# Optimization experiments

Hardware: AMD Instinct MI355X
Metric: run time of the kernel (lower is better)

Reference implementation:

```python
import jax, jax.numpy as jnp
import numpy as np

BS = 8        # number of batched graphs (paired point clouds, must be even)
NPTS = 16384  # points per graph (equal-size graphs -> segment ops are per-row softmax)
C = 32        # feature channels
CG = 8        # global feature channels from pooling head
K = 256
KNN = 16      # key_mean_num neighbors


def setup_inputs() -> dict:
    key = jax.random.key(0)
    ks = jax.random.split(key, 5)
    N = BS * NPTS
    return {
        "feature": jax.random.normal(ks[0], (N, C, 1), dtype=jnp.float32),
        "pos": jax.random.normal(ks[1], (N, 3), dtype=jnp.float32),
        "W_pool": jax.random.normal(ks[2], (C, 1 + CG), dtype=jnp.float32) / np.float32(np.sqrt(C)),
        "W_regress": jax.random.normal(ks[3], (3 * C + 2 * CG, K), dtype=jnp.float32) / np.float32(np.sqrt(3 * C + 2 * CG)),
        "W_extract": jax.random.normal(ks[4], (C, C), dtype=jnp.float32) / np.float32(np.sqrt(C)),
        "bs": BS,
    }


def reference(feature, pos, W_pool, W_regress, W_extract, bs):
    N, Cc, _ = feature.shape
    n = N // bs
    f = feature.reshape(bs, n, Cc)          # [bs, n, C] (deg-0 fiber, D=1)
    pos_b = pos.reshape(bs, n, 3)

    # --- global pooling head: per-graph segment softmax (dgl.softmax_nodes) ---
    logits = jnp.einsum('bnc,cl->bnl', f, W_pool)      # [bs, n, 1+Cg]
    prob = jax.nn.softmax(logits[..., 0], axis=1)      # [bs, n] pooling weights
    batched = jnp.einsum('bnc,bn->bc', f, prob)        # dgl.sum_nodes weighted -> [bs, C]
    glob = jnp.einsum('bnl,bn->bl', logits[..., 1:], prob)  # [bs, Cg]

    # --- cat_0 cross-pair global merge (tensor_1 <-> tensor_2 swap) ---
    h = bs // 2
    extra = jnp.concatenate([jnp.concatenate([glob[:h], glob[h:]], 1),
                             jnp.concatenate([glob[h:], glob[:h]], 1)], 0)     # [bs, 2Cg]
    paired = jnp.concatenate([jnp.concatenate([batched[:h], batched[h:]], 1),
                              jnp.concatenate([batched[h:], batched[:h]], 1)], 0)  # [bs, 2C]
    f_new = jnp.concatenate([
        f,
        jnp.broadcast_to(extra[:, None, :], (bs, n, extra.shape[1])),   # broadcast_nodes
        jnp.broadcast_to(paired[:, None, :], (bs, n, paired.shape[1])),
    ], axis=-1)                                                          # [bs, n, 3C+2Cg]

    pw = jax.nn.softmax(jnp.einsum('bnc,ck->bnk', f_new, W_regress), axis=1)  # [bs, n, K]
    keypoints = jnp.einsum('bnk,bnd->bkd', pw, pos_b)                         # [bs, K, 3]

    # --- batched KNN: k nearest source points per keypoint, within graph ---
    d2 = jnp.sum((keypoints[:, :, None, :] - pos_b[:, None, :, :]) ** 2, axis=-1)  # [bs, K, n]
    _, idx = jax.lax.top_k(-d2, KNN)                                               # [bs, K, k]

    # --- bipartite gather + keypoint feature extraction (mean aggregate + linear) ---
    neigh = jax.vmap(lambda fb, ib: fb[ib])(f, idx)   # [bs, K, k, C]
    pooled = neigh.mean(axis=2)                        # [bs, K, C]
    return jnp.einsum('bkc,co->bko', pooled, W_extract)  # key_tensor [bs, K, C]
```

## Files before the change

### kernel.cpp

```cpp
#include <hip/hip_runtime.h>
#include <math.h>

#define BS 8
#define NPTS 16384
#define C 32
#define K 256
#define KNNK 16
#define NBINS 512
#define BINW 0.00025f
#define CAP 4096
#define NSPL 64

typedef float f32x4 __attribute__((ext_vector_type(4)));
typedef __bf16 bf16x8 __attribute__((ext_vector_type(8)));
union U16x8 { int4 i; bf16x8 v; unsigned short u[8]; };

__global__ __launch_bounds__(256, 2) void k_logits(
    const float* __restrict__ f, const float* __restrict__ pos,
    const float* __restrict__ Wr, float* __restrict__ partials) {
  int b = blockIdx.x >> 6;
  int r = blockIdx.x & 63;
  int pbase = b * NPTS + r * 256;
  int t = threadIdx.x;
  int w = t >> 6, lane = t & 63;
  int h = w & 1, nh = w >> 1;
  int quad = lane >> 4, col = lane & 15;

  __shared__ float4 posLDS[256];
  __shared__ float4 fm[2][256];

  float* rawf = (float*)&fm[0][0];
  if (t < 192) ((float4*)rawf)[t] = ((const float4*)(pos + (size_t)pbase * 3))[t];
  __syncthreads();
  float4 myp = make_float4(rawf[t * 3], rawf[t * 3 + 1], rawf[t * 3 + 2], 0.f);
  __syncthreads();
  posLDS[t] = myp;

  U16x8 Bh[8], Bl[8];
#pragma unroll
  for (int jt = 0; jt < 8; jt++) {
    int tile = h * 8 + jt;
#pragma unroll
    for (int j = 0; j < 8; j++) {
      float v = Wr[(quad * 8 + j) * K + tile * 16 + col];
      unsigned u = __float_as_uint(v);
      unsigned hb = u >> 16;
      float hf = __uint_as_float(hb << 16);
      unsigned lb = __float_as_uint(v - hf) >> 16;
      Bh[jt].u[j] = (unsigned short)hb;
      Bl[jt].u[j] = (unsigned short)lb;
    }
  }
  float acce[8], accx[8], accy[8], accz[8];
#pragma unroll
  for (int jt = 0; jt < 8; jt++) { acce[jt] = 0.f; accx[jt] = 0.f; accy[jt] = 0.f; accz[jt] = 0.f; }

#pragma unroll 1
  for (int nt = nh * 8; nt < nh * 8 + 8; nt++) {
    const float* fb = f + ((size_t)(pbase + nt * 16 + col)) * C + quad * 8;
    float4 a0 = *(const float4*)fb;
    float4 a1 = *(const float4*)(fb + 4);
    float av[8] = {a0.x, a0.y, a0.z, a0.w, a1.x, a1.y, a1.z, a1.w};
    U16x8 Ah, Al;
#pragma unroll
    for (int j = 0; j < 8; j++) {
      unsigned u = __float_as_uint(av[j]);
      unsigned hb = u >> 16;
      float hf = __uint_as_float(hb << 16);
      unsigned lb = __float_as_uint(av[j] - hf) >> 16;
      Ah.u[j] = (unsigned short)hb;
      Al.u[j] = (unsigned short)lb;
    }
    float4 pr0 = posLDS[nt * 16 + quad * 4 + 0];
    float4 pr1 = posLDS[nt * 16 + quad * 4 + 1];
    float4 pr2 = posLDS[nt * 16 + quad * 4 + 2];
    float4 pr3 = posLDS[nt * 16 + quad * 4 + 3];
#pragma unroll
    for (int jt = 0; jt < 8; jt++) {
      f32x4 d = {0.f, 0.f, 0.f, 0.f};
      d = __builtin_amdgcn_mfma_f32_16x16x32_bf16(Al.v, Bh[jt].v, d, 0, 0, 0);
      d = __builtin_amdgcn_mfma_f32_16x16x32_bf16(Ah.v, Bl[jt].v, d, 0, 0, 0);
      d = __builtin_amdgcn_mfma_f32_16x16x32_bf16(Ah.v, Bh[jt].v, d, 0, 0, 0);
      float e0 = __expf(d[0]), e1 = __expf(d[1]), e2 = __expf(d[2]), e3 = __expf(d[3]);
      acce[jt] += (e0 + e1) + (e2 + e3);
      accx[jt] += e0 * pr0.x + e1 * pr1.x + e2 * pr2.x + e3 * pr3.x;
      accy[jt] += e0 * pr0.y + e1 * pr1.y + e2 * pr2.y + e3 * pr3.y;
      accz[jt] += e0 * pr0.z + e1 * pr1.z + e2 * pr2.z + e3 * pr3.z;
    }
  }

#pragma unroll
  for (int jt = 0; jt < 8; jt++) {
    acce[jt] += __shfl_xor(acce[jt], 16); acce[jt] += __shfl_xor(acce[jt], 32);
    accx[jt] += __shfl_xor(accx[jt], 16); accx[jt] += __shfl_xor(accx[jt], 32);
    accy[jt] += __shfl_xor(accy[jt], 16); accy[jt] += __shfl_xor(accy[jt], 32);
    accz[jt] += __shfl_xor(accz[jt], 16); accz[jt] += __shfl_xor(accz[jt], 32);
  }
  __syncthreads();
  if (lane < 16) {
#pragma unroll
    for (int jt = 0; jt < 8; jt++)
      fm[nh][h * 128 + jt * 16 + lane] = make_float4(acce[jt], accx[jt], accy[jt], accz[jt]);
  }
  __syncthreads();
  float4 v0 = fm[0][t], v1 = fm[1][t];
  float4* po = (float4*)partials;
  po[(size_t)blockIdx.x * 256 + t] =
      make_float4(v0.x + v1.x, v0.y + v1.y, v0.z + v1.z, v0.w + v1.w);
}

__global__ __launch_bounds__(1024) void k_graph(
    const float* __restrict__ pos, const float* __restrict__ partials,
    int* __restrict__ knn) {
  int b = blockIdx.x;
  int t = threadIdx.x;
  int lane = t & 63, wave = t >> 6;

  __shared__ float4 mred[4][256];
  __shared__ float kxs[256], kys[256], kzs[256];
  __shared__ float wred[16][3];
  __shared__ float bc[6];
  __shared__ unsigned hist[NBINS];
  __shared__ unsigned lcnt, ovf;
  __shared__ float cxs[CAP], cys[CAP], czs[CAP];
  __shared__ int cis[CAP];

  {
    int kp = t & 255, q = t >> 8;
    const float4* po = (const float4*)partials;
    float sl = 0.f, sx = 0.f, sy = 0.f, sz = 0.f;
#pragma unroll 4
    for (int j = 0; j < 16; j++) {
      float4 v = po[((size_t)(b * NSPL + q * 16 + j)) * 256 + kp];
      sl += v.x; sx += v.y; sy += v.z; sz += v.w;
    }
    mred[q][kp] = make_float4(sl, sx, sy, sz);
  }
  for (int i = t; i < NBINS; i += 1024) hist[i] = 0;
  if (t == 0) { lcnt = 0; ovf = 0; }
  __syncthreads();
  if (t < 256) {
    float4 a0 = mred[0][t], a1 = mred[1][t], a2 = mred[2][t], a3 = mred[3][t];
    float L = (a0.x + a1.x) + (a2.x + a3.x);
    float inv = 1.f / L;
    kxs[t] = ((a0.y + a1.y) + (a2.y + a3.y)) * inv;
    kys[t] = ((a0.z + a1.z) + (a2.z + a3.z)) * inv;
    kzs[t] = ((a0.w + a1.w) + (a2.w + a3.w)) * inv;
  }
  __syncthreads();

  float sx = 0.f, sy = 0.f, sz = 0.f;
  if (t < 256) { sx = kxs[t]; sy = kys[t]; sz = kzs[t]; }
#pragma unroll
  for (int off = 32; off; off >>= 1) {
    sx += __shfl_xor(sx, off, 64);
    sy += __shfl_xor(sy, off, 64);
    sz += __shfl_xor(sz, off, 64);
  }
  if (lane == 0) { wred[wave][0] = sx; wred[wave][1] = sy; wred[wave][2] = sz; }
  __syncthreads();
  if (t == 0) {
    float X = 0.f, Y = 0.f, Z = 0.f;
#pragma unroll
    for (int i = 0; i < 16; i++) { X += wred[i][0]; Y += wred[i][1]; Z += wred[i][2]; }
    bc[0] = X / K; bc[1] = Y / K; bc[2] = Z / K;
  }
  __syncthreads();
  float cx = bc[0], cy = bc[1], cz = bc[2];
  float md = 0.f;
  if (t < 256) {
    float dx = kxs[t] - cx, dy = kys[t] - cy, dz = kzs[t] - cz;
    md = dx * dx + dy * dy + dz * dz;
  }
#pragma unroll
  for (int off = 32; off; off >>= 1) md = fmaxf(md, __shfl_xor(md, off, 64));
  if (lane == 0) wred[wave][0] = md;
  __syncthreads();
  if (t == 0) {
    float m = 0.f;
#pragma unroll
    for (int i = 0; i < 16; i++) m = fmaxf(m, wred[i][0]);
    bc[3] = sqrtf(m);
  }
  __syncthreads();

#pragma unroll 4
  for (int i = 0; i < 16; i++) {
    int p = b * NPTS + i * 1024 + t;
    float dx = pos[p * 3 + 0] - cx, dy = pos[p * 3 + 1] - cy, dz = pos[p * 3 + 2] - cz;
    float d2 = dx * dx + dy * dy + dz * dz;
    int bin = (int)(d2 * (1.0f / BINW));
    if (bin < NBINS - 1) atomicAdd(&hist[bin], 1u);
  }
  __syncthreads();

  if (t == 0) {
    unsigned cum = 0; float T2 = -1.f;
    for (int i = 0; i < NBINS - 1; i++) {
      cum += hist[i];
      if (cum >= KNNK) { T2 = (i + 1) * BINW; break; }
    }
    if (T2 < 0.f) bc[4] = 3.0e38f;
    else {
      float Rf = sqrtf(T2) + 2.f * bc[3];
      bc[4] = Rf * Rf;
    }
  }
  __syncthreads();
  float r2 = bc[4];

#pragma unroll 4
  for (int i = 0; i < 16; i++) {
    int pl = i * 1024 + t;
    int p = b * NPTS + pl;
    float px = pos[p * 3 + 0], py = pos[p * 3 + 1], pz = pos[p * 3 + 2];
    float dx = px - cx, dy = py - cy, dz = pz - cz;
    float d2 = dx * dx + dy * dy + dz * dz;
    if (d2 <= r2) {
      unsigned u = atomicAdd(&lcnt, 1u);
      if (u < CAP) { cxs[u] = px; cys[u] = py; czs[u] = pz; cis[u] = pl; }
      else ovf = 1;
    }
  }
  __syncthreads();

  if (t < 256) {
    float kx = kxs[t], ky = kys[t], kz = kzs[t];
    float dd[KNNK]; int ii[KNNK];
#pragma unroll
    for (int j = 0; j < KNNK; j++) { dd[j] = 1e30f; ii[j] = 0; }
    float mx = 1e30f;
    if (!ovf) {
      int n = (int)lcnt;
      for (int j = 0; j < n; j++) {
        float dx = kx - cxs[j], dy = ky - cys[j], dz = kz - czs[j];
        float d2 = dx * dx + dy * dy + dz * dz;
        if (d2 < mx) {
          int sm = 0; float bv = dd[0];
#pragma unroll
          for (int s = 1; s < KNNK; s++) if (dd[s] > bv) { bv = dd[s]; sm = s; }
#pragma unroll
          for (int s = 0; s < KNNK; s++) if (s == sm) { dd[s] = d2; ii[s] = cis[j]; }
          mx = dd[0];
#pragma unroll
          for (int s = 1; s < KNNK; s++) mx = fmaxf(mx, dd[s]);
        }
      }
    } else {
      for (int j = 0; j < NPTS; j++) {
        const float* pp = pos + (size_t)(b * NPTS + j) * 3;
        float dx = kx - pp[0], dy = ky - pp[1], dz = kz - pp[2];
        float d2 = dx * dx + dy * dy + dz * dz;
        if (d2 < mx) {
          int sm = 0; float bv = dd[0];
#pragma unroll
          for (int s = 1; s < KNNK; s++) if (dd[s] > bv) { bv = dd[s]; sm = s; }
#pragma unroll
          for (int s = 0; s < KNNK; s++) if (s == sm) { dd[s] = d2; ii[s] = j; }
          mx = dd[0];
#pragma unroll
          for (int s = 1; s < KNNK; s++) mx = fmaxf(mx, dd[s]);
        }
      }
    }
    for (int j = 0; j < KNNK; j++) knn[((size_t)(b * K + t)) * KNNK + j] = ii[j];
  }
}

__global__ __launch_bounds__(256) void k_extract(
    const float* __restrict__ f, const int* __restrict__ knn,
    const float* __restrict__ We, float* __restrict__ out) {
  __shared__ float P[8][C + 1];
  int tid = threadIdx.x;
  int kp = tid >> 5, c = tid & 31;
  int gk = blockIdx.x * 8 + kp;
  int b = gk >> 8;
  float s = 0.f;
#pragma unroll
  for (int j = 0; j < KNNK; j++) {
    int pl = knn[(size_t)gk * KNNK + j];
    s += f[((size_t)(b * NPTS + pl)) * C + c];
  }
  P[kp][c] = s * (1.f / KNNK);
  __syncthreads();
  float r = 0.f;
#pragma unroll
  for (int cc = 0; cc < C; cc++) r += P[kp][cc] * We[cc * C + c];
  out[(size_t)gk * C + c] = r;
}

extern "C" void kernel_launch(void* const* d_in, const int* in_sizes, int n_in,
                              void* d_out, int out_size, void* d_ws, size_t ws_size,
                              hipStream_t stream) {
  const float* f   = (const float*)d_in[0];
  const float* pos = (const float*)d_in[1];
  const float* Wr  = (const float*)d_in[3];
  const float* We  = (const float*)d_in[4];
  float* out = (float*)d_out;

  char* ws = (char*)d_ws;
  float* partials = (float*)(ws + 0);
  int*   knn      = (int*)(ws + (size_t)2 * 1024 * 1024);

  k_logits <<<dim3(BS * NSPL), dim3(256),  0, stream>>>(f, pos, Wr, partials);
  k_graph  <<<dim3(BS),        dim3(1024), 0, stream>>>(pos, partials, knn);
  k_extract<<<dim3(256),       dim3(256),  0, stream>>>(f, knn, We, out);
}
```

Before: 132.8 us.

## Split monolithic graph kernel into merge, histogram, compaction and top-k kernels

The single 8-block k_graph kernel becomes four kernels. Keypoint merging stays at 8 blocks, the distance histogram and candidate compaction now run on 64 blocks each through global atomics, and the top-k scan runs per graph with 256 threads. The goal is to spread the pos-scanning phases across more CUs instead of 8 workgroups. In exchange it adds three launches, global atomic contention, and a round trip for the candidate list through global memory.

```diff
diff --git a/kernel.cpp b/kernel.cpp
--- a/kernel.cpp
+++ b/kernel.cpp
@@ -109,9 +109,10 @@
       make_float4(v0.x + v1.x, v0.y + v1.y, v0.z + v1.z, v0.w + v1.w);
 }
 
-__global__ __launch_bounds__(1024) void k_graph(
-    const float* __restrict__ pos, const float* __restrict__ partials,
-    int* __restrict__ knn) {
+__global__ __launch_bounds__(1024) void k_merge(
+    const float* __restrict__ partials, float* __restrict__ kpts,
+    float* __restrict__ gstat, unsigned* __restrict__ ghist,
+    unsigned* __restrict__ ccnt) {
   int b = blockIdx.x;
   int t = threadIdx.x;
   int lane = t & 63, wave = t >> 6;
@@ -119,33 +120,32 @@
   __shared__ float4 mred[4][256];
   __shared__ float kxs[256], kys[256], kzs[256];
   __shared__ float wred[16][3];
-  __shared__ float bc[6];
-  __shared__ unsigned hist[NBINS];
-  __shared__ unsigned lcnt, ovf;
-  __shared__ float cxs[CAP], cys[CAP], czs[CAP];
-  __shared__ int cis[CAP];
+  __shared__ float bc[4];
+
+  if (t < NBINS) ghist[b * NBINS + t] = 0;
+  if (t == 0) ccnt[b] = 0;
 
   {
     int kp = t & 255, q = t >> 8;
     const float4* po = (const float4*)partials;
     float sl = 0.f, sx = 0.f, sy = 0.f, sz = 0.f;
-#pragma unroll 4
+#pragma unroll
     for (int j = 0; j < 16; j++) {
       float4 v = po[((size_t)(b * NSPL + q * 16 + j)) * 256 + kp];
       sl += v.x; sx += v.y; sy += v.z; sz += v.w;
     }
     mred[q][kp] = make_float4(sl, sx, sy, sz);
   }
-  for (int i = t; i < NBINS; i += 1024) hist[i] = 0;
-  if (t == 0) { lcnt = 0; ovf = 0; }
   __syncthreads();
   if (t < 256) {
     float4 a0 = mred[0][t], a1 = mred[1][t], a2 = mred[2][t], a3 = mred[3][t];
     float L = (a0.x + a1.x) + (a2.x + a3.x);
     float inv = 1.f / L;
-    kxs[t] = ((a0.y + a1.y) + (a2.y + a3.y)) * inv;
-    kys[t] = ((a0.z + a1.z) + (a2.z + a3.z)) * inv;
-    kzs[t] = ((a0.w + a1.w) + (a2.w + a3.w)) * inv;
+    float x = ((a0.y + a1.y) + (a2.y + a3.y)) * inv;
+    float y = ((a0.z + a1.z) + (a2.z + a3.z)) * inv;
+    float z = ((a0.w + a1.w) + (a2.w + a3.w)) * inv;
+    kxs[t] = x; kys[t] = y; kzs[t] = z;
+    ((float4*)kpts)[b * 256 + t] = make_float4(x, y, z, 0.f);
   }
   __syncthreads();
 
@@ -167,6 +167,7 @@
   }
   __syncthreads();
   float cx = bc[0], cy = bc[1], cz = bc[2];
+
   float md = 0.f;
   if (t < 256) {
     float dx = kxs[t] - cx, dy = kys[t] - cy, dz = kzs[t] - cz;
@@ -180,91 +181,133 @@
     float m = 0.f;
 #pragma unroll
     for (int i = 0; i < 16; i++) m = fmaxf(m, wred[i][0]);
-    bc[3] = sqrtf(m);
-  }
-  __syncthreads();
-
-#pragma unroll 4
-  for (int i = 0; i < 16; i++) {
-    int p = b * NPTS + i * 1024 + t;
-    float dx = pos[p * 3 + 0] - cx, dy = pos[p * 3 + 1] - cy, dz = pos[p * 3 + 2] - cz;
+    ((float4*)gstat)[b] = make_float4(cx, cy, cz, sqrtf(m));
+  }
+}
+
+__global__ __launch_bounds__(256) void k_hist(
+    const float* __restrict__ pos, const float* __restrict__ gstat,
+    unsigned* __restrict__ ghist) {
+  int b = blockIdx.x >> 3;
+  int ch = blockIdx.x & 7;
+  int t = threadIdx.x;
+  __shared__ unsigned hist[NBINS];
+  hist[t] = 0; hist[t + 256] = 0;
+  float4 st = ((const float4*)gstat)[b];
+  __syncthreads();
+  int base = b * NPTS + ch * 2048;
+#pragma unroll
+  for (int i = 0; i < 8; i++) {
+    int p = base + i * 256 + t;
+    float dx = pos[p * 3 + 0] - st.x, dy = pos[p * 3 + 1] - st.y, dz = pos[p * 3 + 2] - st.z;
     float d2 = dx * dx + dy * dy + dz * dz;
     int bin = (int)(d2 * (1.0f / BINW));
     if (bin < NBINS - 1) atomicAdd(&hist[bin], 1u);
   }
   __syncthreads();
-
+  unsigned v0 = hist[t], v1 = hist[t + 256];
+  if (v0) atomicAdd(&ghist[b * NBINS + t], v0);
+  if (v1) atomicAdd(&ghist[b * NBINS + t + 256], v1);
+}
+
+__global__ __launch_bounds__(256) void k_compact(
+    const float* __restrict__ pos, const float* __restrict__ gstat,
+    const unsigned* __restrict__ ghist, unsigned* __restrict__ ccnt,
+    float4* __restrict__ cand) {
+  int b = blockIdx.x >> 3;
+  int ch = blockIdx.x & 7;
+  int t = threadIdx.x;
+  __shared__ unsigned hist[NBINS];
+  __shared__ float shr2;
+  hist[t] = ghist[b * NBINS + t];
+  hist[t + 256] = ghist[b * NBINS + t + 256];
+  float4 st = ((const float4*)gstat)[b];
+  __syncthreads();
   if (t == 0) {
     unsigned cum = 0; float T2 = -1.f;
     for (int i = 0; i < NBINS - 1; i++) {
       cum += hist[i];
       if (cum >= KNNK) { T2 = (i + 1) * BINW; break; }
     }
-    if (T2 < 0.f) bc[4] = 3.0e38f;
+    if (T2 < 0.f) shr2 = 3.0e38f;
     else {
-      float Rf = sqrtf(T2) + 2.f * bc[3];
-      bc[4] = Rf * Rf;
-    }
-  }
-  __syncthreads();
-  float r2 = bc[4];
-
-#pragma unroll 4
-  for (int i = 0; i < 16; i++) {
-    int pl = i * 1024 + t;
+      float Rf = sqrtf(T2) + 2.f * st.w;
+      shr2 = Rf * Rf;
+    }
+  }
+  __syncthreads();
+  float r2 = shr2;
+#pragma unroll
+  for (int i = 0; i < 8; i++) {
+    int pl = ch * 2048 + i * 256 + t;
     int p = b * NPTS + pl;
     float px = pos[p * 3 + 0], py = pos[p * 3 + 1], pz = pos[p * 3 + 2];
-    float dx = px - cx, dy = py - cy, dz = pz - cz;
+    float dx = px - st.x, dy = py - st.y, dz = pz - st.z;
     float d2 = dx * dx + dy * dy + dz * dz;
     if (d2 <= r2) {
-      unsigned u = atomicAdd(&lcnt, 1u);
-      if (u < CAP) { cxs[u] = px; cys[u] = py; czs[u] = pz; cis[u] = pl; }
-      else ovf = 1;
-    }
-  }
-  __syncthreads();
-
-  if (t < 256) {
-    float kx = kxs[t], ky = kys[t], kz = kzs[t];
-    float dd[KNNK]; int ii[KNNK];
-#pragma unroll
-    for (int j = 0; j < KNNK; j++) { dd[j] = 1e30f; ii[j] = 0; }
-    float mx = 1e30f;
-    if (!ovf) {
-      int n = (int)lcnt;
-      for (int j = 0; j < n; j++) {
-        float dx = kx - cxs[j], dy = ky - cys[j], dz = kz - czs[j];
-        float d2 = dx * dx + dy * dy + dz * dz;
-        if (d2 < mx) {
-          int sm = 0; float bv = dd[0];
-#pragma unroll
-          for (int s = 1; s < KNNK; s++) if (dd[s] > bv) { bv = dd[s]; sm = s; }
-#pragma unroll
-          for (int s = 0; s < KNNK; s++) if (s == sm) { dd[s] = d2; ii[s] = cis[j]; }
-          mx = dd[0];
-#pragma unroll
-          for (int s = 1; s < KNNK; s++) mx = fmaxf(mx, dd[s]);
-        }
+      unsigned u = atomicAdd(&ccnt[b], 1u);
+      if (u < CAP) cand[(size_t)b * CAP + u] = make_float4(px, py, pz, __int_as_float(pl));
+    }
+  }
+}
+
+__global__ __launch_bounds__(256) void k_topk(
+    const float* __restrict__ pos, const float* __restrict__ kpts,
+    const unsigned* __restrict__ ccnt, const float4* __restrict__ cand,
+    int* __restrict__ knn) {
+  int b = blockIdx.x;
+  int t = threadIdx.x;
+  __shared__ float cxs[CAP], cys[CAP], czs[CAP];
+  __shared__ int cis[CAP];
+
+  unsigned cnt = ccnt[b];
+  int ovf = cnt > CAP;
+  int n = ovf ? 0 : (int)cnt;
+  for (int j = t; j < n; j += 256) {
+    float4 v = cand[(size_t)b * CAP + j];
+    cxs[j] = v.x; cys[j] = v.y; czs[j] = v.z; cis[j] = __float_as_int(v.w);
+  }
+  __syncthreads();
+
+  float4 kpt = ((const float4*)kpts)[b * 256 + t];
+  float kx = kpt.x, ky = kpt.y, kz = kpt.z;
+  float dd[KNNK]; int ii[KNNK];
+#pragma unroll
+  for (int j = 0; j < KNNK; j++) { dd[j] = 1e30f; ii[j] = 0; }
+  float mx = 1e30f;
+  if (!ovf) {
+    for (int j = 0; j < n; j++) {
+      float dx = kx - cxs[j], dy = ky - cys[j], dz = kz - czs[j];
+      float d2 = dx * dx + dy * dy + dz * dz;
+      if (d2 < mx) {
+        int sm = 0; float bv = dd[0];
+#pragma unroll
+        for (int s = 1; s < KNNK; s++) if (dd[s] > bv) { bv = dd[s]; sm = s; }
+#pragma unroll
+        for (int s = 0; s < KNNK; s++) if (s == sm) { dd[s] = d2; ii[s] = cis[j]; }
+        mx = dd[0];
+#pragma unroll
+        for (int s = 1; s < KNNK; s++) mx = fmaxf(mx, dd[s]);
       }
-    } else {
-      for (int j = 0; j < NPTS; j++) {
-        const float* pp = pos + (size_t)(b * NPTS + j) * 3;
-        float dx = kx - pp[0], dy = ky - pp[1], dz = kz - pp[2];
-        float d2 = dx * dx + dy * dy + dz * dz;
-        if (d2 < mx) {
-          int sm = 0; float bv = dd[0];
-#pragma unroll
-          for (int s = 1; s < KNNK; s++) if (dd[s] > bv) { bv = dd[s]; sm = s; }
-#pragma unroll
-          for (int s = 0; s < KNNK; s++) if (s == sm) { dd[s] = d2; ii[s] = j; }
-          mx = dd[0];
-#pragma unroll
-          for (int s = 1; s < KNNK; s++) mx = fmaxf(mx, dd[s]);
-        }
+    }
+  } else {
+    for (int j = 0; j < NPTS; j++) {
+      const float* pp = pos + (size_t)(b * NPTS + j) * 3;
+      float dx = kx - pp[0], dy = ky - pp[1], dz = kz - pp[2];
+      float d2 = dx * dx + dy * dy + dz * dz;
+      if (d2 < mx) {
+        int sm = 0; float bv = dd[0];
+#pragma unroll
+        for (int s = 1; s < KNNK; s++) if (dd[s] > bv) { bv = dd[s]; sm = s; }
+#pragma unroll
+        for (int s = 0; s < KNNK; s++) if (s == sm) { dd[s] = d2; ii[s] = j; }
+        mx = dd[0];
+#pragma unroll
+        for (int s = 1; s < KNNK; s++) mx = fmaxf(mx, dd[s]);
       }
     }
-    for (int j = 0; j < KNNK; j++) knn[((size_t)(b * K + t)) * KNNK + j] = ii[j];
-  }
+  }
+  for (int j = 0; j < KNNK; j++) knn[((size_t)(b * K + t)) * KNNK + j] = ii[j];
 }
 
 __global__ __launch_bounds__(256) void k_extract(
@@ -299,10 +342,18 @@
   float* out = (float*)d_out;
 
   char* ws = (char*)d_ws;
-  float* partials = (float*)(ws + 0);
-  int*   knn      = (int*)(ws + (size_t)2 * 1024 * 1024);
+  float*    partials = (float*)(ws + 0);
+  int*      knn      = (int*)(ws + 2097152);
+  float*    kpts     = (float*)(ws + 2228224);
+  float*    gstat    = (float*)(ws + 2260992);
+  unsigned* ghist    = (unsigned*)(ws + 2261504);
+  unsigned* ccnt     = (unsigned*)(ws + 2277888);
+  float4*   cand     = (float4*)(ws + 2278016);
 
   k_logits <<<dim3(BS * NSPL), dim3(256),  0, stream>>>(f, pos, Wr, partials);
-  k_graph  <<<dim3(BS),        dim3(1024), 0, stream>>>(pos, partials, knn);
+  k_merge  <<<dim3(BS),        dim3(1024), 0, stream>>>(partials, kpts, gstat, ghist, ccnt);
+  k_hist   <<<dim3(BS * 8),    dim3(256),  0, stream>>>(pos, gstat, ghist);
+  k_compact<<<dim3(BS * 8),    dim3(256),  0, stream>>>(pos, gstat, ghist, ccnt, cand);
+  k_topk   <<<dim3(BS),        dim3(256),  0, stream>>>(pos, kpts, ccnt, cand, knn);
   k_extract<<<dim3(256),       dim3(256),  0, stream>>>(f, knn, We, out);
 }
```

New measurement: 131.2 us. No clear change (-1.2%).

## Merge graph and extract stages into one cooperative kernel spread over 128 blocks

Applied to the files above, without the earlier changes.

Replaces the 8-block k_graph and the separate k_extract with one cooperative kernel of 16 blocks per graph, using grid.sync between phases. Keypoint reduction, histogram, candidate filtering and KNN are split so that each block handles 16 keypoints and a slice of points, with global atomics for histograms and candidate counts. Feature gather and projection are fused at the end. The aim is to remove the serial single-block-per-graph bottleneck and one launch, at the cost of grid-wide barriers and global-memory candidate lists instead of shared memory.

```diff
diff --git a/kernel.cpp b/kernel.cpp
--- a/kernel.cpp
+++ b/kernel.cpp
@@ -1,5 +1,8 @@
 #include <hip/hip_runtime.h>
+#include <hip/hip_cooperative_groups.h>
 #include <math.h>
+
+namespace cg = cooperative_groups;
 
 #define BS 8
 #define NPTS 16384
@@ -109,138 +112,165 @@
       make_float4(v0.x + v1.x, v0.y + v1.y, v0.z + v1.z, v0.w + v1.w);
 }
 
-__global__ __launch_bounds__(1024) void k_graph(
-    const float* __restrict__ pos, const float* __restrict__ partials,
-    int* __restrict__ knn) {
-  int b = blockIdx.x;
+__global__ __launch_bounds__(256) void k_coop(
+    const float* __restrict__ pos, const float* __restrict__ f,
+    const float* __restrict__ We, const float* __restrict__ partials,
+    float* __restrict__ kpts, float* __restrict__ gstat,
+    unsigned* __restrict__ ghist, unsigned* __restrict__ ccnt,
+    float4* __restrict__ cand, float* __restrict__ out) {
+  cg::grid_group grid = cg::this_grid();
+  int blk = blockIdx.x;
+  int g = blk >> 4;
+  int sb = blk & 15;
   int t = threadIdx.x;
   int lane = t & 63, wave = t >> 6;
 
-  __shared__ float4 mred[4][256];
-  __shared__ float kxs[256], kys[256], kzs[256];
-  __shared__ float wred[16][3];
-  __shared__ float bc[6];
+  __shared__ float4 red[16][17];
+  __shared__ float bc[4];
+  __shared__ float wred[4][4];
   __shared__ unsigned hist[NBINS];
-  __shared__ unsigned lcnt, ovf;
-  __shared__ float cxs[CAP], cys[CAP], czs[CAP];
-  __shared__ int cis[CAP];
+  __shared__ unsigned sc[NBINS];
+  __shared__ int mbin;
+  __shared__ int nidx[16][KNNK];
+  __shared__ float P[16][C + 1];
+
+  if (t < 32) ghist[blk * 32 + t] = 0;
+  if (blk == 0 && t < BS) ccnt[t] = 0;
 
   {
-    int kp = t & 255, q = t >> 8;
+    int kpl = t & 15, sg = t >> 4;
     const float4* po = (const float4*)partials;
-    float sl = 0.f, sx = 0.f, sy = 0.f, sz = 0.f;
-#pragma unroll 4
-    for (int j = 0; j < 16; j++) {
-      float4 v = po[((size_t)(b * NSPL + q * 16 + j)) * 256 + kp];
-      sl += v.x; sx += v.y; sy += v.z; sz += v.w;
-    }
-    mred[q][kp] = make_float4(sl, sx, sy, sz);
-  }
-  for (int i = t; i < NBINS; i += 1024) hist[i] = 0;
-  if (t == 0) { lcnt = 0; ovf = 0; }
-  __syncthreads();
-  if (t < 256) {
-    float4 a0 = mred[0][t], a1 = mred[1][t], a2 = mred[2][t], a3 = mred[3][t];
-    float L = (a0.x + a1.x) + (a2.x + a3.x);
+    int kp = sb * 16 + kpl;
+    float4 s = make_float4(0.f, 0.f, 0.f, 0.f);
+#pragma unroll
+    for (int k2 = 0; k2 < 4; k2++) {
+      float4 v = po[((size_t)(g * NSPL + sg + k2 * 16)) * 256 + kp];
+      s.x += v.x; s.y += v.y; s.z += v.z; s.w += v.w;
+    }
+    red[sg][kpl] = s;
+  }
+  __syncthreads();
+  if (t < 16) {
+    float L = 0.f, x = 0.f, y = 0.f, z = 0.f;
+#pragma unroll
+    for (int sg = 0; sg < 16; sg++) {
+      float4 v = red[sg][t];
+      L += v.x; x += v.y; y += v.z; z += v.w;
+    }
     float inv = 1.f / L;
-    kxs[t] = ((a0.y + a1.y) + (a2.y + a3.y)) * inv;
-    kys[t] = ((a0.z + a1.z) + (a2.z + a3.z)) * inv;
-    kzs[t] = ((a0.w + a1.w) + (a2.w + a3.w)) * inv;
-  }
-  __syncthreads();
-
-  float sx = 0.f, sy = 0.f, sz = 0.f;
-  if (t < 256) { sx = kxs[t]; sy = kys[t]; sz = kzs[t]; }
-#pragma unroll
-  for (int off = 32; off; off >>= 1) {
-    sx += __shfl_xor(sx, off, 64);
-    sy += __shfl_xor(sy, off, 64);
-    sz += __shfl_xor(sz, off, 64);
-  }
-  if (lane == 0) { wred[wave][0] = sx; wred[wave][1] = sy; wred[wave][2] = sz; }
-  __syncthreads();
-  if (t == 0) {
-    float X = 0.f, Y = 0.f, Z = 0.f;
-#pragma unroll
-    for (int i = 0; i < 16; i++) { X += wred[i][0]; Y += wred[i][1]; Z += wred[i][2]; }
-    bc[0] = X / K; bc[1] = Y / K; bc[2] = Z / K;
-  }
-  __syncthreads();
-  float cx = bc[0], cy = bc[1], cz = bc[2];
-  float md = 0.f;
-  if (t < 256) {
-    float dx = kxs[t] - cx, dy = kys[t] - cy, dz = kzs[t] - cz;
-    md = dx * dx + dy * dy + dz * dz;
-  }
-#pragma unroll
-  for (int off = 32; off; off >>= 1) md = fmaxf(md, __shfl_xor(md, off, 64));
-  if (lane == 0) wred[wave][0] = md;
-  __syncthreads();
-  if (t == 0) {
-    float m = 0.f;
-#pragma unroll
-    for (int i = 0; i < 16; i++) m = fmaxf(m, wred[i][0]);
-    bc[3] = sqrtf(m);
-  }
-  __syncthreads();
-
-#pragma unroll 4
-  for (int i = 0; i < 16; i++) {
-    int p = b * NPTS + i * 1024 + t;
-    float dx = pos[p * 3 + 0] - cx, dy = pos[p * 3 + 1] - cy, dz = pos[p * 3 + 2] - cz;
-    float d2 = dx * dx + dy * dy + dz * dz;
-    int bin = (int)(d2 * (1.0f / BINW));
+    ((float4*)kpts)[g * 256 + sb * 16 + t] = make_float4(x * inv, y * inv, z * inv, 0.f);
+  }
+  grid.sync();
+
+  if (sb == 0) {
+    float4 kpt = ((const float4*)kpts)[g * 256 + t];
+    float sx = kpt.x, sy = kpt.y, sz = kpt.z;
+#pragma unroll
+    for (int off = 32; off; off >>= 1) {
+      sx += __shfl_xor(sx, off, 64);
+      sy += __shfl_xor(sy, off, 64);
+      sz += __shfl_xor(sz, off, 64);
+    }
+    if (lane == 0) { wred[wave][0] = sx; wred[wave][1] = sy; wred[wave][2] = sz; }
+    __syncthreads();
+    if (t == 0) {
+      float X = 0.f, Y = 0.f, Z = 0.f;
+#pragma unroll
+      for (int i = 0; i < 4; i++) { X += wred[i][0]; Y += wred[i][1]; Z += wred[i][2]; }
+      bc[0] = X / K; bc[1] = Y / K; bc[2] = Z / K;
+    }
+    __syncthreads();
+    float cx = bc[0], cy = bc[1], cz = bc[2];
+    float dx = kpt.x - cx, dy = kpt.y - cy, dz = kpt.z - cz;
+    float md = dx * dx + dy * dy + dz * dz;
+#pragma unroll
+    for (int off = 32; off; off >>= 1) md = fmaxf(md, __shfl_xor(md, off, 64));
+    if (lane == 0) wred[wave][3] = md;
+    __syncthreads();
+    if (t == 0) {
+      float m = fmaxf(fmaxf(wred[0][3], wred[1][3]), fmaxf(wred[2][3], wred[3][3]));
+      ((float4*)gstat)[g] = make_float4(cx, cy, cz, sqrtf(m));
+    }
+  }
+  grid.sync();
+
+  float4 st = ((const float4*)gstat)[g];
+  hist[t] = 0; hist[t + 256] = 0;
+  __syncthreads();
+  float px[4], py[4], pz[4], pd[4];
+#pragma unroll
+  for (int i = 0; i < 4; i++) {
+    int pl = sb * 1024 + i * 256 + t;
+    const float* pp = pos + (size_t)(g * NPTS + pl) * 3;
+    px[i] = pp[0]; py[i] = pp[1]; pz[i] = pp[2];
+    float dx = px[i] - st.x, dy = py[i] - st.y, dz = pz[i] - st.z;
+    pd[i] = dx * dx + dy * dy + dz * dz;
+    int bin = (int)(pd[i] * (1.0f / BINW));
     if (bin < NBINS - 1) atomicAdd(&hist[bin], 1u);
   }
   __syncthreads();
-
-  if (t == 0) {
-    unsigned cum = 0; float T2 = -1.f;
-    for (int i = 0; i < NBINS - 1; i++) {
-      cum += hist[i];
-      if (cum >= KNNK) { T2 = (i + 1) * BINW; break; }
-    }
-    if (T2 < 0.f) bc[4] = 3.0e38f;
-    else {
-      float Rf = sqrtf(T2) + 2.f * bc[3];
-      bc[4] = Rf * Rf;
-    }
-  }
-  __syncthreads();
-  float r2 = bc[4];
-
-#pragma unroll 4
-  for (int i = 0; i < 16; i++) {
-    int pl = i * 1024 + t;
-    int p = b * NPTS + pl;
-    float px = pos[p * 3 + 0], py = pos[p * 3 + 1], pz = pos[p * 3 + 2];
-    float dx = px - cx, dy = py - cy, dz = pz - cz;
-    float d2 = dx * dx + dy * dy + dz * dz;
-    if (d2 <= r2) {
-      unsigned u = atomicAdd(&lcnt, 1u);
-      if (u < CAP) { cxs[u] = px; cys[u] = py; czs[u] = pz; cis[u] = pl; }
-      else ovf = 1;
-    }
-  }
-  __syncthreads();
-
-  if (t < 256) {
-    float kx = kxs[t], ky = kys[t], kz = kzs[t];
+  {
+    unsigned v0 = hist[t], v1 = hist[t + 256];
+    if (v0) atomicAdd(&ghist[g * NBINS + t], v0);
+    if (v1) atomicAdd(&ghist[g * NBINS + t + 256], v1);
+  }
+  grid.sync();
+
+  sc[t] = ghist[g * NBINS + t];
+  sc[t + 256] = ghist[g * NBINS + t + 256];
+  if (t == 0) mbin = NBINS - 1;
+  __syncthreads();
+  for (int off = 1; off < NBINS; off <<= 1) {
+    unsigned a0 = (t >= off) ? sc[t - off] : 0u;
+    unsigned a1 = ((t + 256) >= off) ? sc[t + 256 - off] : 0u;
+    __syncthreads();
+    sc[t] += a0; sc[t + 256] += a1;
+    __syncthreads();
+  }
+  {
+    unsigned c0 = sc[t], p0 = t ? sc[t - 1] : 0u;
+    unsigned c1 = sc[t + 256], p1 = sc[t + 255];
+    if (c0 >= KNNK && p0 < KNNK) atomicMin(&mbin, t);
+    if ((t + 256) < (NBINS - 1) && c1 >= KNNK && p1 < KNNK) atomicMin(&mbin, t + 256);
+  }
+  __syncthreads();
+  float r2;
+  if (mbin < NBINS - 1) {
+    float Rf = sqrtf((mbin + 1) * BINW) + 2.f * st.w;
+    r2 = Rf * Rf;
+  } else r2 = 3.0e38f;
+
+#pragma unroll
+  for (int i = 0; i < 4; i++) {
+    if (pd[i] <= r2) {
+      int pl = sb * 1024 + i * 256 + t;
+      unsigned u = atomicAdd(&ccnt[g], 1u);
+      if (u < CAP) cand[(size_t)g * CAP + u] = make_float4(px[i], py[i], pz[i], __int_as_float(pl));
+    }
+  }
+  grid.sync();
+
+  unsigned cnt = ccnt[g];
+  int ovf = cnt > CAP;
+  if (t < 16) {
+    float4 kpt = ((const float4*)kpts)[g * 256 + sb * 16 + t];
+    float kx = kpt.x, ky = kpt.y, kz = kpt.z;
     float dd[KNNK]; int ii[KNNK];
 #pragma unroll
     for (int j = 0; j < KNNK; j++) { dd[j] = 1e30f; ii[j] = 0; }
     float mx = 1e30f;
     if (!ovf) {
-      int n = (int)lcnt;
+      int n = (int)cnt;
       for (int j = 0; j < n; j++) {
-        float dx = kx - cxs[j], dy = ky - cys[j], dz = kz - czs[j];
+        float4 v = cand[(size_t)g * CAP + j];
+        float dx = kx - v.x, dy = ky - v.y, dz = kz - v.z;
         float d2 = dx * dx + dy * dy + dz * dz;
         if (d2 < mx) {
           int sm = 0; float bv = dd[0];
 #pragma unroll
           for (int s = 1; s < KNNK; s++) if (dd[s] > bv) { bv = dd[s]; sm = s; }
 #pragma unroll
-          for (int s = 0; s < KNNK; s++) if (s == sm) { dd[s] = d2; ii[s] = cis[j]; }
+          for (int s = 0; s < KNNK; s++) if (s == sm) { dd[s] = d2; ii[s] = __float_as_int(v.w); }
           mx = dd[0];
 #pragma unroll
           for (int s = 1; s < KNNK; s++) mx = fmaxf(mx, dd[s]);
@@ -248,7 +278,7 @@
       }
     } else {
       for (int j = 0; j < NPTS; j++) {
-        const float* pp = pos + (size_t)(b * NPTS + j) * 3;
+        const float* pp = pos + (size_t)(g * NPTS + j) * 3;
         float dx = kx - pp[0], dy = ky - pp[1], dz = kz - pp[2];
         float d2 = dx * dx + dy * dy + dz * dz;
         if (d2 < mx) {
@@ -263,30 +293,34 @@
         }
       }
     }
-    for (int j = 0; j < KNNK; j++) knn[((size_t)(b * K + t)) * KNNK + j] = ii[j];
-  }
-}
-
-__global__ __launch_bounds__(256) void k_extract(
-    const float* __restrict__ f, const int* __restrict__ knn,
-    const float* __restrict__ We, float* __restrict__ out) {
-  __shared__ float P[8][C + 1];
-  int tid = threadIdx.x;
-  int kp = tid >> 5, c = tid & 31;
-  int gk = blockIdx.x * 8 + kp;
-  int b = gk >> 8;
-  float s = 0.f;
-#pragma unroll
-  for (int j = 0; j < KNNK; j++) {
-    int pl = knn[(size_t)gk * KNNK + j];
-    s += f[((size_t)(b * NPTS + pl)) * C + c];
-  }
-  P[kp][c] = s * (1.f / KNNK);
-  __syncthreads();
-  float r = 0.f;
-#pragma unroll
-  for (int cc = 0; cc < C; cc++) r += P[kp][cc] * We[cc * C + c];
-  out[(size_t)gk * C + c] = r;
+#pragma unroll
+    for (int j = 0; j < KNNK; j++) nidx[t][j] = ii[j];
+  }
+  __syncthreads();
+
+  {
+    int c = t & 31, kl = t >> 5;
+#pragma unroll
+    for (int hh = 0; hh < 2; hh++) {
+      int kp = kl + hh * 8;
+      float s = 0.f;
+#pragma unroll
+      for (int j = 0; j < KNNK; j++) {
+        int pl = nidx[kp][j];
+        s += f[((size_t)(g * NPTS + pl)) * C + c];
+      }
+      P[kp][c] = s * (1.f / KNNK);
+    }
+    __syncthreads();
+#pragma unroll
+    for (int hh = 0; hh < 2; hh++) {
+      int kp = kl + hh * 8;
+      float r = 0.f;
+#pragma unroll
+      for (int cc = 0; cc < C; cc++) r += P[kp][cc] * We[cc * C + c];
+      out[((size_t)(g * K + sb * 16 + kp)) * C + c] = r;
+    }
+  }
 }
 
 extern "C" void kernel_launch(void* const* d_in, const int* in_sizes, int n_in,
@@ -299,10 +333,18 @@
   float* out = (float*)d_out;
 
   char* ws = (char*)d_ws;
-  float* partials = (float*)(ws + 0);
-  int*   knn      = (int*)(ws + (size_t)2 * 1024 * 1024);
-
-  k_logits <<<dim3(BS * NSPL), dim3(256),  0, stream>>>(f, pos, Wr, partials);
-  k_graph  <<<dim3(BS),        dim3(1024), 0, stream>>>(pos, partials, knn);
-  k_extract<<<dim3(256),       dim3(256),  0, stream>>>(f, knn, We, out);
+  float*    partials = (float*)(ws + 0);
+  float*    kpts     = (float*)(ws + 2097152);
+  float*    gstat    = (float*)(ws + 2129920);
+  unsigned* ghist    = (unsigned*)(ws + 2130432);
+  unsigned* ccnt     = (unsigned*)(ws + 2146816);
+  float4*   cand     = (float4*)(ws + 2147072);
+
+  k_logits<<<dim3(BS * NSPL), dim3(256), 0, stream>>>(f, pos, Wr, partials);
+
+  void* args[] = {(void*)&pos, (void*)&f, (void*)&We, (void*)&partials,
+                  (void*)&kpts, (void*)&gstat, (void*)&ghist, (void*)&ccnt,
+                  (void*)&cand, (void*)&out};
+  hipLaunchCooperativeKernel((const void*)k_coop, dim3(BS * 16), dim3(256),
+                             args, 0, stream);
 }
```

After: 180.3 us. 35.8% more time.
